# Optimization experiments

Measured on AMD Instinct MI355X. Metric: run time of the kernel, lower is better.

## Reference

```python
import jax, jax.numpy as jnp
import numpy as np

B, LQ, LKV, D = 8, 2048, 2048, 1024

def setup_inputs() -> dict:
    key = jax.random.key(0)
    k1, k2, k3, k4, k5, k6, k7 = jax.random.split(key, 7)
    s = 1.0 / np.sqrt(D)
    return {
        "query": jax.random.normal(k1, (B, LQ, D), jnp.float32),
        "key": jax.random.normal(k2, (B, LKV, D), jnp.float32),
        "value": jax.random.normal(k3, (B, LKV, D), jnp.float32),
        "Wq": jax.random.uniform(k4, (D, D), jnp.float32, -s, s),
        "bq": jax.random.uniform(k5, (D,), jnp.float32, -s, s),
        "Wk": jax.random.uniform(k6, (D, D), jnp.float32, -s, s),
        "bk": jax.random.uniform(k7, (D,), jnp.float32, -s, s),
        "scale_factor": 32,
        "dropout_p": 0,
    }

def reference(query, key, value, Wq, bq, Wk, bk, scale_factor, dropout_p):
    # q/k linear projections (torch Linear: x @ W^T + b); v is used raw per the source
    q = jnp.einsum("bld,ed->ble", query, Wq) + bq
    k = jnp.einsum("bld,ed->ble", key, Wk) + bk
    scores = jnp.einsum("bqd,bkd->bqk", q, k) / jnp.float32(scale_factor)
    attn = jax.nn.softmax(scores, axis=-1)
    # dropout_p == 0 -> identity (deterministic baseline)
    return jnp.einsum("bqk,bkd->bqd", attn, value)
```

## Files before the change

kernel.cpp:

```cpp
#include <hip/hip_runtime.h>

typedef __bf16 bf16;
typedef __attribute__((ext_vector_type(4))) __bf16 bf16x4;
typedef __attribute__((ext_vector_type(8))) __bf16 bf16x8;
typedef __attribute__((ext_vector_type(4))) float f32x4;

__device__ __forceinline__ void gload_lds16(const void* g, void* l) {
  __builtin_amdgcn_global_load_lds(
      (const __attribute__((address_space(1))) unsigned int*)(unsigned long long)g,
      (__attribute__((address_space(3))) unsigned int*)(unsigned long long)l,
      16, 0, 0);
}

__global__ void cast_f32_bf16(const float* __restrict__ in, bf16* __restrict__ out, int n4) {
  int i = blockIdx.x * blockDim.x + threadIdx.x;
  if (i >= n4) return;
  float4 v = reinterpret_cast<const float4*>(in)[i];
  bf16x4 o;
  o[0] = (bf16)v.x; o[1] = (bf16)v.y; o[2] = (bf16)v.z; o[3] = (bf16)v.w;
  reinterpret_cast<bf16x4*>(out)[i] = o;
}

__global__ void transpose_cast(const float* __restrict__ V, bf16* __restrict__ VT,
                               int rows, int cols) {
  __shared__ bf16 tile[64][65];
  const int b = blockIdx.z;
  const float* Vb = V + (long)b * rows * cols;
  bf16* VTb = VT + (long)b * rows * cols;
  const int d0 = blockIdx.x * 64;
  const int k0 = blockIdx.y * 64;
  const int t = threadIdx.x;
  const int r = t >> 4;
  const int c4 = (t & 15) * 4;
#pragma unroll
  for (int p = 0; p < 4; ++p) {
    float4 v = *reinterpret_cast<const float4*>(&Vb[(long)(k0 + p * 16 + r) * cols + d0 + c4]);
    tile[p * 16 + r][c4 + 0] = (bf16)v.x;
    tile[p * 16 + r][c4 + 1] = (bf16)v.y;
    tile[p * 16 + r][c4 + 2] = (bf16)v.z;
    tile[p * 16 + r][c4 + 3] = (bf16)v.w;
  }
  __syncthreads();
#pragma unroll
  for (int p = 0; p < 4; ++p) {
    const int dd = p * 16 + r;
    bf16x4 o;
    o[0] = tile[c4 + 0][dd];
    o[1] = tile[c4 + 1][dd];
    o[2] = tile[c4 + 2][dd];
    o[3] = tile[c4 + 3][dd];
    *reinterpret_cast<bf16x4*>(&VTb[(long)(d0 + dd) * rows + k0 + c4]) = o;
  }
}

__global__ void softmax_rows(bf16* __restrict__ S) {
  const long row = blockIdx.x;
  bf16* p = S + row * 2048;
  const int t = threadIdx.x;
  const int wid = t >> 6;
  const int lane = t & 63;
  bf16x8 v = *reinterpret_cast<bf16x8*>(p + t * 8);
  float f[8];
  float m = -3.0e38f;
#pragma unroll
  for (int j = 0; j < 8; ++j) { f[j] = (float)v[j]; m = fmaxf(m, f[j]); }
#pragma unroll
  for (int off = 32; off >= 1; off >>= 1) m = fmaxf(m, __shfl_xor(m, off));
  __shared__ float redm[4], reds[4];
  if (lane == 0) redm[wid] = m;
  __syncthreads();
  m = fmaxf(fmaxf(redm[0], redm[1]), fmaxf(redm[2], redm[3]));
  float s = 0.f;
#pragma unroll
  for (int j = 0; j < 8; ++j) { f[j] = __expf(f[j] - m); s += f[j]; }
#pragma unroll
  for (int off = 32; off >= 1; off >>= 1) s += __shfl_xor(s, off);
  if (lane == 0) reds[wid] = s;
  __syncthreads();
  s = reds[0] + reds[1] + reds[2] + reds[3];
  const float inv = 1.0f / s;
  bf16x8 o;
#pragma unroll
  for (int j = 0; j < 8; ++j) o[j] = (bf16)(f[j] * inv);
  *reinterpret_cast<bf16x8*>(p + t * 8) = o;
}

template <int MODE>
__global__ void gemm_bt(const bf16* __restrict__ A, const bf16* __restrict__ Bm,
                        const float* __restrict__ bias, void* __restrict__ Cvoid,
                        const int* __restrict__ scale_ptr,
                        int M, int N, int K, long sA, long sB, long sC) {
  __shared__ bf16 Alds[128][32];
  __shared__ bf16 Blds[128][32];
  const int t = threadIdx.x;
  const int lane = t & 63;
  const int wid = t >> 6;
  const int wm = wid >> 1;
  const int wn = wid & 1;

  const int gx = gridDim.x, gy = gridDim.y;
  const int nwg = gx * gy * gridDim.z;
  int id = blockIdx.x + gx * (blockIdx.y + gy * blockIdx.z);
  if ((nwg & 7) == 0) {
    const int cpx = nwg >> 3;
    id = (id & 7) * cpx + (id >> 3);
  }
  const int bx = id % gx;
  const int by = (id / gx) % gy;
  const int bz = id / (gx * gy);

  const bf16* Ab = A + (long)bz * sA;
  const bf16* Bb = Bm + (long)bz * sB;
  const int tile_m = by * 128;
  const int tile_n = bx * 128;

  const int r0 = t >> 2;
  const int kc0 = t & 3;
  const int sk = (kc0 ^ ((r0 >> 1) & 3)) * 8;
  const bf16* gA0 = Ab + (long)(tile_m + r0) * K + sk;
  const bf16* gA1 = gA0 + (long)64 * K;
  const bf16* gB0 = Bb + (long)(tile_n + r0) * K + sk;
  const bf16* gB1 = gB0 + (long)64 * K;
  bf16* lA0 = &Alds[0][0] + wid * 512;
  bf16* lA1 = lA0 + 2048;
  bf16* lB0 = &Blds[0][0] + wid * 512;
  bf16* lB1 = lB0 + 2048;

  const int frow = lane & 15;
  const int fkc = lane >> 4;
  const int pko = (fkc ^ ((frow >> 1) & 3)) * 8;
  const bf16* aFrag = &Alds[wm * 64 + frow][pko];
  const bf16* bFrag = &Blds[wn * 64 + frow][pko];

  f32x4 acc[4][4] = {};
  const int nk = K >> 5;
  for (int kt = 0; kt < nk; ++kt) {
    const int ko = kt * 32;
    gload_lds16(gA0 + ko, lA0);
    gload_lds16(gA1 + ko, lA1);
    gload_lds16(gB0 + ko, lB0);
    gload_lds16(gB1 + ko, lB1);
    __syncthreads();
    bf16x8 af[4], bfv[4];
#pragma unroll
    for (int i = 0; i < 4; ++i) {
      af[i] = *reinterpret_cast<const bf16x8*>(aFrag + i * 512);
      bfv[i] = *reinterpret_cast<const bf16x8*>(bFrag + i * 512);
    }
#pragma unroll
    for (int mi = 0; mi < 4; ++mi)
#pragma unroll
      for (int ni = 0; ni < 4; ++ni)
        acc[mi][ni] = __builtin_amdgcn_mfma_f32_16x16x32_bf16(af[mi], bfv[ni], acc[mi][ni], 0, 0, 0);
    __syncthreads();
  }

  float scl = 1.0f;
  if (MODE == 1) {
    const int iv = scale_ptr[0];
    const float fv = __int_as_float(iv);
    const float sv = (iv > 0 && iv < (1 << 20)) ? (float)iv : fv;
    scl = 1.0f / sv;
  }
  const int rb = tile_m + wm * 64 + ((lane >> 4) << 2);
  const int cb = tile_n + wn * 64 + (lane & 15);
  if (MODE == 2) {
    float* C = reinterpret_cast<float*>(Cvoid) + (long)bz * sC;
#pragma unroll
    for (int mi = 0; mi < 4; ++mi)
#pragma unroll
      for (int ni = 0; ni < 4; ++ni)
#pragma unroll
        for (int r = 0; r < 4; ++r)
          C[(long)(rb + mi * 16 + r) * N + (cb + ni * 16)] = acc[mi][ni][r];
  } else {
    bf16* C = reinterpret_cast<bf16*>(Cvoid) + (long)bz * sC;
#pragma unroll
    for (int ni = 0; ni < 4; ++ni) {
      const int col = cb + ni * 16;
      const float bv = (MODE == 0) ? bias[col] : 0.0f;
#pragma unroll
      for (int mi = 0; mi < 4; ++mi)
#pragma unroll
        for (int r = 0; r < 4; ++r)
          C[(long)(rb + mi * 16 + r) * N + col] = (bf16)(acc[mi][ni][r] * scl + bv);
    }
  }
}

extern "C" void kernel_launch(void* const* d_in, const int* in_sizes, int n_in,
                              void* d_out, int out_size, void* d_ws, size_t ws_size,
                              hipStream_t stream) {
  (void)in_sizes; (void)n_in; (void)out_size; (void)ws_size;
  const float* query = (const float*)d_in[0];
  const float* key   = (const float*)d_in[1];
  const float* value = (const float*)d_in[2];
  const float* Wq    = (const float*)d_in[3];
  const float* bq    = (const float*)d_in[4];
  const float* Wk    = (const float*)d_in[5];
  const float* bk    = (const float*)d_in[6];
  const int*   scale = (const int*)d_in[7];

  const int L = 2048, D = 1024;
  char* ws = (char*)d_ws;
  bf16* q_cast = (bf16*)ws;
  bf16* k_cast = q_cast + (long)16384 * 1024;
  bf16* S      = q_cast;
  bf16* Qp     = (bf16*)(ws + (size_t)67108864);
  bf16* Kp     = (bf16*)(ws + (size_t)100663296);
  bf16* VT     = (bf16*)(ws + (size_t)134217728);
  bf16* Wqb    = (bf16*)(ws + (size_t)167772160);
  bf16* Wkb    = (bf16*)(ws + (size_t)169869312);

  cast_f32_bf16<<<16384, 256, 0, stream>>>(query, q_cast, 4194304);
  cast_f32_bf16<<<16384, 256, 0, stream>>>(key,   k_cast, 4194304);
  cast_f32_bf16<<<1024,  256, 0, stream>>>(Wq, Wqb, 262144);
  cast_f32_bf16<<<1024,  256, 0, stream>>>(Wk, Wkb, 262144);
  transpose_cast<<<dim3(16, 32, 8), 256, 0, stream>>>(value, VT, 2048, 1024);

  gemm_bt<0><<<dim3(8, 128, 1), 256, 0, stream>>>(q_cast, Wqb, bq, Qp, nullptr,
                                                  16384, 1024, 1024, 0, 0, 0);
  gemm_bt<0><<<dim3(8, 128, 1), 256, 0, stream>>>(k_cast, Wkb, bk, Kp, nullptr,
                                                  16384, 1024, 1024, 0, 0, 0);
  gemm_bt<1><<<dim3(16, 16, 8), 256, 0, stream>>>(Qp, Kp, nullptr, S, scale,
                                                  2048, 2048, 1024,
                                                  (long)L * D, (long)L * D, (long)L * L);
  softmax_rows<<<16384, 256, 0, stream>>>(S);
  gemm_bt<2><<<dim3(8, 16, 8), 256, 0, stream>>>(S, VT, nullptr, d_out, nullptr,
                                                 2048, 1024, 2048,
                                                 (long)L * L, (long)D * L, (long)L * D);
}
```

Measured before the change: 324.3 us.

## Rewrite GEMM as 256x256 double-buffered pipelined kernel with 8 waves

Replaces the single-buffered 128x128x32 GEMM with a 256x256x64 tile using 512 threads, double-buffered LDS, and direct global-to-LDS async loads. The loads for the next k-tile are interleaved between quarters of the MFMA work, with explicit barriers, waitcnt and setprio. The goal is to hide global load latency behind compute and to raise arithmetic intensity per LDS byte. In exchange it uses 128KB of LDS per block and a large accumulator register footprint, which may limit occupancy. The grid swizzle now assumes the block count is divisible by 8.

After: 289.0 us. 1.12x faster.

```diff
diff --git a/kernel.cpp b/kernel.cpp
--- a/kernel.cpp
+++ b/kernel.cpp
@@ -85,23 +85,82 @@
   *reinterpret_cast<bf16x8*>(p + t * 8) = o;
 }
 
+
+#define BARRIER __builtin_amdgcn_s_barrier()
+#define LGKM0                                              \
+  do {                                                     \
+    asm volatile("s_waitcnt lgkmcnt(0)" ::: "memory");     \
+    __builtin_amdgcn_sched_barrier(0);                     \
+  } while (0)
+#define VM0                                                \
+  do {                                                     \
+    asm volatile("s_waitcnt vmcnt(0)" ::: "memory");       \
+    __builtin_amdgcn_sched_barrier(0);                     \
+  } while (0)
+
+#define STAGE_A(buf, ko)                                        \
+  {                                                             \
+    bf16* l_ = ldsd + (buf) * 32768;                            \
+    const bf16* g_ = gA + (ko);                                 \
+    gload_lds16(g_, l_);                                        \
+    gload_lds16(g_ + rK64, l_ + 4096);                          \
+    gload_lds16(g_ + rK128, l_ + 8192);                         \
+    gload_lds16(g_ + rK128 + rK64, l_ + 12288);                 \
+  }
+#define STAGE_B(buf, ko)                                        \
+  {                                                             \
+    bf16* l_ = ldsd + (buf) * 32768 + 16384;                    \
+    const bf16* g_ = gB + (ko);                                 \
+    gload_lds16(g_, l_);                                        \
+    gload_lds16(g_ + rK64, l_ + 4096);                          \
+    gload_lds16(g_ + rK128, l_ + 8192);                         \
+    gload_lds16(g_ + rK128 + rK64, l_ + 12288);                 \
+  }
+
+#define LOADA(buf, mq)                                                        \
+  {                                                                           \
+    const bf16* p_ = aBase + (buf) * 32768 + (mq) * 4096;                     \
+    _Pragma("unroll") for (int m_ = 0; m_ < 4; ++m_) {                        \
+      a[m_][0] = *reinterpret_cast<const bf16x8*>(p_ + m_ * 1024 + pk0);      \
+      a[m_][1] = *reinterpret_cast<const bf16x8*>(p_ + m_ * 1024 + pk1);      \
+    }                                                                         \
+  }
+#define LOADB(buf, nq)                                                        \
+  {                                                                           \
+    const bf16* p_ = bBase + (buf) * 32768 + (nq) * 2048;                     \
+    _Pragma("unroll") for (int n_ = 0; n_ < 2; ++n_) {                        \
+      b[(nq) * 2 + n_][0] = *reinterpret_cast<const bf16x8*>(p_ + n_ * 1024 + pk0); \
+      b[(nq) * 2 + n_][1] = *reinterpret_cast<const bf16x8*>(p_ + n_ * 1024 + pk1); \
+    }                                                                         \
+  }
+
+#define MFMAQ(mq, nq)                                                         \
+  _Pragma("unroll") for (int m_ = 0; m_ < 4; ++m_)                            \
+  _Pragma("unroll") for (int n_ = 0; n_ < 2; ++n_)                            \
+  _Pragma("unroll") for (int ks_ = 0; ks_ < 2; ++ks_)                         \
+      acc[(mq) * 4 + m_][(nq) * 2 + n_] =                                     \
+          __builtin_amdgcn_mfma_f32_16x16x32_bf16(                            \
+              a[m_][ks_], b[(nq) * 2 + n_][ks_],                              \
+              acc[(mq) * 4 + m_][(nq) * 2 + n_], 0, 0, 0);
+
 template <int MODE>
-__global__ void gemm_bt(const bf16* __restrict__ A, const bf16* __restrict__ Bm,
-                        const float* __restrict__ bias, void* __restrict__ Cvoid,
-                        const int* __restrict__ scale_ptr,
-                        int M, int N, int K, long sA, long sB, long sC) {
-  __shared__ bf16 Alds[128][32];
-  __shared__ bf16 Blds[128][32];
+__global__ __launch_bounds__(512, 2)
+void gemm_bt(const bf16* __restrict__ A, const bf16* __restrict__ Bm,
+             const float* __restrict__ bias, void* __restrict__ Cvoid,
+             const int* __restrict__ scale_ptr,
+             int M, int N, int K, long sA, long sB, long sC) {
+  __shared__ bf16 lds[2][2][2][128][64];
   const int t = threadIdx.x;
   const int lane = t & 63;
   const int wid = t >> 6;
-  const int wm = wid >> 1;
-  const int wn = wid & 1;
+  const int wm = wid >> 2;
+  const int wn = wid & 3;
+  (void)M;
 
   const int gx = gridDim.x, gy = gridDim.y;
   const int nwg = gx * gy * gridDim.z;
   int id = blockIdx.x + gx * (blockIdx.y + gy * blockIdx.z);
-  if ((nwg & 7) == 0) {
+  {
     const int cpx = nwg >> 3;
     id = (id & 7) * cpx + (id >> 3);
   }
@@ -111,49 +170,74 @@
 
   const bf16* Ab = A + (long)bz * sA;
   const bf16* Bb = Bm + (long)bz * sB;
-  const int tile_m = by * 128;
-  const int tile_n = bx * 128;
-
-  const int r0 = t >> 2;
-  const int kc0 = t & 3;
-  const int sk = (kc0 ^ ((r0 >> 1) & 3)) * 8;
-  const bf16* gA0 = Ab + (long)(tile_m + r0) * K + sk;
-  const bf16* gA1 = gA0 + (long)64 * K;
-  const bf16* gB0 = Bb + (long)(tile_n + r0) * K + sk;
-  const bf16* gB1 = gB0 + (long)64 * K;
-  bf16* lA0 = &Alds[0][0] + wid * 512;
-  bf16* lA1 = lA0 + 2048;
-  bf16* lB0 = &Blds[0][0] + wid * 512;
-  bf16* lB1 = lB0 + 2048;
+  const int tile_m = by * 256;
+  const int tile_n = bx * 256;
+
+  const int srow = t >> 3;
+  const int skc = t & 7;
+  const int soff = ((skc ^ (srow & 7)) << 3);
+  const bf16* gA = Ab + (long)(tile_m + srow) * K + soff;
+  const bf16* gB = Bb + (long)(tile_n + srow) * K + soff;
+  const long rK64 = (long)K << 6;
+  const long rK128 = (long)K << 7;
+  bf16* const ldsd = &lds[0][0][0][0][0] + wid * 512;
 
   const int frow = lane & 15;
-  const int fkc = lane >> 4;
-  const int pko = (fkc ^ ((frow >> 1) & 3)) * 8;
-  const bf16* aFrag = &Alds[wm * 64 + frow][pko];
-  const bf16* bFrag = &Blds[wn * 64 + frow][pko];
-
-  f32x4 acc[4][4] = {};
-  const int nk = K >> 5;
-  for (int kt = 0; kt < nk; ++kt) {
-    const int ko = kt * 32;
-    gload_lds16(gA0 + ko, lA0);
-    gload_lds16(gA1 + ko, lA1);
-    gload_lds16(gB0 + ko, lB0);
-    gload_lds16(gB1 + ko, lB1);
-    __syncthreads();
-    bf16x8 af[4], bfv[4];
-#pragma unroll
-    for (int i = 0; i < 4; ++i) {
-      af[i] = *reinterpret_cast<const bf16x8*>(aFrag + i * 512);
-      bfv[i] = *reinterpret_cast<const bf16x8*>(bFrag + i * 512);
-    }
-#pragma unroll
-    for (int mi = 0; mi < 4; ++mi)
-#pragma unroll
-      for (int ni = 0; ni < 4; ++ni)
-        acc[mi][ni] = __builtin_amdgcn_mfma_f32_16x16x32_bf16(af[mi], bfv[ni], acc[mi][ni], 0, 0, 0);
-    __syncthreads();
-  }
+  const int pk0 = (((lane >> 4) ^ (lane & 7))) << 3;
+  const int pk1 = (((4 | (lane >> 4)) ^ (lane & 7))) << 3;
+  const bf16* aBase = &lds[0][0][wm][frow][0];
+  const bf16* bBase = &lds[0][1][wn >> 1][(wn & 1) * 64 + frow][0];
+
+  bf16x8 a[4][2], b[4][2];
+  f32x4 acc[8][4] = {};
+
+  STAGE_A(0, 0)
+  STAGE_B(0, 0)
+  VM0;
+  BARRIER;
+
+  const int NK = K >> 6;
+  int c = 0;
+  for (int kt = 0; kt < NK - 1; ++kt, c ^= 1) {
+    const long ko = (long)(kt + 1) << 6;
+    LOADA(c, 0)
+    LOADB(c, 0)
+    STAGE_A(c ^ 1, ko)
+    BARRIER;
+    LGKM0;
+    __builtin_amdgcn_s_setprio(1);
+    MFMAQ(0, 0)
+    __builtin_amdgcn_s_setprio(0);
+    BARRIER;
+    LOADB(c, 1)
+    STAGE_B(c ^ 1, ko)
+    BARRIER;
+    LGKM0;
+    __builtin_amdgcn_s_setprio(1);
+    MFMAQ(0, 1)
+    __builtin_amdgcn_s_setprio(0);
+    BARRIER;
+    LOADA(c, 1)
+    BARRIER;
+    LGKM0;
+    __builtin_amdgcn_s_setprio(1);
+    MFMAQ(1, 0)
+    __builtin_amdgcn_s_setprio(0);
+    BARRIER;
+    VM0;
+    BARRIER;
+    __builtin_amdgcn_s_setprio(1);
+    MFMAQ(1, 1)
+    __builtin_amdgcn_s_setprio(0);
+  }
+  LOADA(c, 0)
+  LOADB(c, 0)
+  LOADB(c, 1)
+  MFMAQ(0, 0)
+  MFMAQ(0, 1)
+  LOADA(c, 1)
+  MFMAQ(1, 0)
+  MFMAQ(1, 1)
 
   float scl = 1.0f;
   if (MODE == 1) {
@@ -162,28 +246,28 @@
     const float sv = (iv > 0 && iv < (1 << 20)) ? (float)iv : fv;
     scl = 1.0f / sv;
   }
-  const int rb = tile_m + wm * 64 + ((lane >> 4) << 2);
+  const int rb = tile_m + wm * 128 + ((lane >> 4) << 2);
   const int cb = tile_n + wn * 64 + (lane & 15);
   if (MODE == 2) {
     float* C = reinterpret_cast<float*>(Cvoid) + (long)bz * sC;
 #pragma unroll
-    for (int mi = 0; mi < 4; ++mi)
-#pragma unroll
-      for (int ni = 0; ni < 4; ++ni)
+    for (int mf = 0; mf < 8; ++mf)
+#pragma unroll
+      for (int nf = 0; nf < 4; ++nf)
 #pragma unroll
         for (int r = 0; r < 4; ++r)
-          C[(long)(rb + mi * 16 + r) * N + (cb + ni * 16)] = acc[mi][ni][r];
+          C[(long)(rb + mf * 16 + r) * N + (cb + nf * 16)] = acc[mf][nf][r];
   } else {
     bf16* C = reinterpret_cast<bf16*>(Cvoid) + (long)bz * sC;
 #pragma unroll
-    for (int ni = 0; ni < 4; ++ni) {
-      const int col = cb + ni * 16;
+    for (int nf = 0; nf < 4; ++nf) {
+      const int col = cb + nf * 16;
       const float bv = (MODE == 0) ? bias[col] : 0.0f;
 #pragma unroll
-      for (int mi = 0; mi < 4; ++mi)
+      for (int mf = 0; mf < 8; ++mf)
 #pragma unroll
         for (int r = 0; r < 4; ++r)
-          C[(long)(rb + mi * 16 + r) * N + col] = (bf16)(acc[mi][ni][r] * scl + bv);
+          C[(long)(rb + mf * 16 + r) * N + col] = (bf16)(acc[mf][nf][r] * scl + bv);
     }
   }
 }
@@ -218,15 +302,15 @@
   cast_f32_bf16<<<1024,  256, 0, stream>>>(Wk, Wkb, 262144);
   transpose_cast<<<dim3(16, 32, 8), 256, 0, stream>>>(value, VT, 2048, 1024);
 
-  gemm_bt<0><<<dim3(8, 128, 1), 256, 0, stream>>>(q_cast, Wqb, bq, Qp, nullptr,
-                                                  16384, 1024, 1024, 0, 0, 0);
-  gemm_bt<0><<<dim3(8, 128, 1), 256, 0, stream>>>(k_cast, Wkb, bk, Kp, nullptr,
-                                                  16384, 1024, 1024, 0, 0, 0);
-  gemm_bt<1><<<dim3(16, 16, 8), 256, 0, stream>>>(Qp, Kp, nullptr, S, scale,
-                                                  2048, 2048, 1024,
-                                                  (long)L * D, (long)L * D, (long)L * L);
+  gemm_bt<0><<<dim3(4, 64, 1), 512, 0, stream>>>(q_cast, Wqb, bq, Qp, nullptr,
+                                                 16384, 1024, 1024, 0, 0, 0);
+  gemm_bt<0><<<dim3(4, 64, 1), 512, 0, stream>>>(k_cast, Wkb, bk, Kp, nullptr,
+                                                 16384, 1024, 1024, 0, 0, 0);
+  gemm_bt<1><<<dim3(8, 8, 8), 512, 0, stream>>>(Qp, Kp, nullptr, S, scale,
+                                                2048, 2048, 1024,
+                                                (long)L * D, (long)L * D, (long)L * L);
   softmax_rows<<<16384, 256, 0, stream>>>(S);
-  gemm_bt<2><<<dim3(8, 16, 8), 256, 0, stream>>>(S, VT, nullptr, d_out, nullptr,
-                                                 2048, 1024, 2048,
-                                                 (long)L * L, (long)D * L, (long)L * D);
-}
+  gemm_bt<2><<<dim3(4, 8, 8), 512, 0, stream>>>(S, VT, nullptr, d_out, nullptr,
+                                                2048, 1024, 2048,
+                                                (long)L * L, (long)D * L, (long)L * D);
+}
```

## Double-buffer LDS in GEMM, widen tile to 128x256, merge Q/K projections

Applied to the files above, without the earlier changes.

The GEMM kernel now uses 512 threads with a 128x256 output tile and double-buffered LDS. The next K-slice is prefetched with global_load_lds while the current one is consumed, so only one barrier remains per iteration. The two separate Q and K projection launches are merged into a single batched launch that picks the bias by batch index. Together these aim to hide global-load latency and raise B-tile reuse, at the cost of more LDS per block (48KB) and possibly lower occupancy.

New measurement: 298.2 us. -8.0%, faster.

```diff
diff --git a/kernel.cpp b/kernel.cpp
--- a/kernel.cpp
+++ b/kernel.cpp
@@ -85,23 +85,46 @@
   *reinterpret_cast<bf16x8*>(p + t * 8) = o;
 }
 
+
+#define STAGE(buf, ko)                          \
+  {                                             \
+    bf16* lA_ = ldsA + (buf) * 12288;           \
+    bf16* lB_ = ldsB + (buf) * 12288;           \
+    gload_lds16(gA + (ko), lA_);                \
+    gload_lds16(gB + (ko), lB_);                \
+    gload_lds16(gB + (ko) + rK128, lB_ + 4096); \
+  }
+
+#define LOADA(buf)                                                             \
+  _Pragma("unroll") for (int m_ = 0; m_ < 4; ++m_)                             \
+      a[m_] = *reinterpret_cast<const bf16x8*>(aB + (buf) * 12288 + m_ * 512);
+#define LOADB(buf)                                                             \
+  _Pragma("unroll") for (int n_ = 0; n_ < 4; ++n_)                             \
+      b[n_] = *reinterpret_cast<const bf16x8*>(bB + (buf) * 12288 + n_ * 512);
+
+#define MFMAP                                                                  \
+  _Pragma("unroll") for (int m_ = 0; m_ < 4; ++m_)                             \
+  _Pragma("unroll") for (int n_ = 0; n_ < 4; ++n_)                             \
+      acc[m_][n_] = __builtin_amdgcn_mfma_f32_16x16x32_bf16(                   \
+          a[m_], b[n_], acc[m_][n_], 0, 0, 0);
+
 template <int MODE>
-__global__ void gemm_bt(const bf16* __restrict__ A, const bf16* __restrict__ Bm,
-                        const float* __restrict__ bias, void* __restrict__ Cvoid,
-                        const int* __restrict__ scale_ptr,
-                        int M, int N, int K, long sA, long sB, long sC) {
-  __shared__ bf16 Alds[128][32];
-  __shared__ bf16 Blds[128][32];
+__global__ __launch_bounds__(512, 4)
+void gemm_bt(const bf16* __restrict__ A, const bf16* __restrict__ Bm,
+             const float* __restrict__ bias0, const float* __restrict__ bias1,
+             void* __restrict__ Cvoid, const int* __restrict__ scale_ptr,
+             int N, int K, long sA, long sB, long sC) {
+  __shared__ bf16 lds[2][12288];
   const int t = threadIdx.x;
   const int lane = t & 63;
   const int wid = t >> 6;
-  const int wm = wid >> 1;
-  const int wn = wid & 1;
+  const int wm = wid >> 2;
+  const int wn = wid & 3;
 
   const int gx = gridDim.x, gy = gridDim.y;
   const int nwg = gx * gy * gridDim.z;
   int id = blockIdx.x + gx * (blockIdx.y + gy * blockIdx.z);
-  if ((nwg & 7) == 0) {
+  {
     const int cpx = nwg >> 3;
     id = (id & 7) * cpx + (id >> 3);
   }
@@ -112,48 +135,39 @@
   const bf16* Ab = A + (long)bz * sA;
   const bf16* Bb = Bm + (long)bz * sB;
   const int tile_m = by * 128;
-  const int tile_n = bx * 128;
-
-  const int r0 = t >> 2;
-  const int kc0 = t & 3;
-  const int sk = (kc0 ^ ((r0 >> 1) & 3)) * 8;
-  const bf16* gA0 = Ab + (long)(tile_m + r0) * K + sk;
-  const bf16* gA1 = gA0 + (long)64 * K;
-  const bf16* gB0 = Bb + (long)(tile_n + r0) * K + sk;
-  const bf16* gB1 = gB0 + (long)64 * K;
-  bf16* lA0 = &Alds[0][0] + wid * 512;
-  bf16* lA1 = lA0 + 2048;
-  bf16* lB0 = &Blds[0][0] + wid * 512;
-  bf16* lB1 = lB0 + 2048;
+  const int tile_n = bx * 256;
+
+  const int srow = t >> 2;
+  const int soff = (((t & 3) ^ ((t >> 3) & 3)) << 3);
+  const bf16* gA = Ab + (long)(tile_m + srow) * K + soff;
+  const bf16* gB = Bb + (long)(tile_n + srow) * K + soff;
+  const long rK128 = (long)K << 7;
+  bf16* const ldsA = &lds[0][0] + wid * 512;
+  bf16* const ldsB = &lds[0][4096] + wid * 512;
 
   const int frow = lane & 15;
-  const int fkc = lane >> 4;
-  const int pko = (fkc ^ ((frow >> 1) & 3)) * 8;
-  const bf16* aFrag = &Alds[wm * 64 + frow][pko];
-  const bf16* bFrag = &Blds[wn * 64 + frow][pko];
-
+  const int pko = (((lane >> 4) ^ ((lane >> 1) & 3)) << 3);
+  const bf16* aB = &lds[0][0] + (wm * 64 + frow) * 32 + pko;
+  const bf16* bB = &lds[0][4096] + (wn * 64 + frow) * 32 + pko;
+
+  bf16x8 a[4], b[4];
   f32x4 acc[4][4] = {};
-  const int nk = K >> 5;
-  for (int kt = 0; kt < nk; ++kt) {
-    const int ko = kt * 32;
-    gload_lds16(gA0 + ko, lA0);
-    gload_lds16(gA1 + ko, lA1);
-    gload_lds16(gB0 + ko, lB0);
-    gload_lds16(gB1 + ko, lB1);
+
+  STAGE(0, 0)
+  __syncthreads();
+
+  const int NK = K >> 5;
+  int c = 0;
+  for (int kt = 0; kt < NK - 1; ++kt, c ^= 1) {
+    STAGE(c ^ 1, (long)(kt + 1) << 5)
+    LOADB(c)
+    LOADA(c)
+    MFMAP
     __syncthreads();
-    bf16x8 af[4], bfv[4];
-#pragma unroll
-    for (int i = 0; i < 4; ++i) {
-      af[i] = *reinterpret_cast<const bf16x8*>(aFrag + i * 512);
-      bfv[i] = *reinterpret_cast<const bf16x8*>(bFrag + i * 512);
-    }
-#pragma unroll
-    for (int mi = 0; mi < 4; ++mi)
-#pragma unroll
-      for (int ni = 0; ni < 4; ++ni)
-        acc[mi][ni] = __builtin_amdgcn_mfma_f32_16x16x32_bf16(af[mi], bfv[ni], acc[mi][ni], 0, 0, 0);
-    __syncthreads();
-  }
+  }
+  LOADB(c)
+  LOADA(c)
+  MFMAP
 
   float scl = 1.0f;
   if (MODE == 1) {
@@ -167,23 +181,24 @@
   if (MODE == 2) {
     float* C = reinterpret_cast<float*>(Cvoid) + (long)bz * sC;
 #pragma unroll
-    for (int mi = 0; mi < 4; ++mi)
-#pragma unroll
-      for (int ni = 0; ni < 4; ++ni)
+    for (int mf = 0; mf < 4; ++mf)
+#pragma unroll
+      for (int nf = 0; nf < 4; ++nf)
 #pragma unroll
         for (int r = 0; r < 4; ++r)
-          C[(long)(rb + mi * 16 + r) * N + (cb + ni * 16)] = acc[mi][ni][r];
+          C[(long)(rb + mf * 16 + r) * N + (cb + nf * 16)] = acc[mf][nf][r];
   } else {
     bf16* C = reinterpret_cast<bf16*>(Cvoid) + (long)bz * sC;
-#pragma unroll
-    for (int ni = 0; ni < 4; ++ni) {
-      const int col = cb + ni * 16;
+    const float* bias = (MODE == 0) ? (bz ? bias1 : bias0) : nullptr;
+#pragma unroll
+    for (int nf = 0; nf < 4; ++nf) {
+      const int col = cb + nf * 16;
       const float bv = (MODE == 0) ? bias[col] : 0.0f;
 #pragma unroll
-      for (int mi = 0; mi < 4; ++mi)
+      for (int mf = 0; mf < 4; ++mf)
 #pragma unroll
         for (int r = 0; r < 4; ++r)
-          C[(long)(rb + mi * 16 + r) * N + col] = (bf16)(acc[mi][ni][r] * scl + bv);
+          C[(long)(rb + mf * 16 + r) * N + col] = (bf16)(acc[mf][nf][r] * scl + bv);
     }
   }
 }
@@ -218,15 +233,14 @@
   cast_f32_bf16<<<1024,  256, 0, stream>>>(Wk, Wkb, 262144);
   transpose_cast<<<dim3(16, 32, 8), 256, 0, stream>>>(value, VT, 2048, 1024);
 
-  gemm_bt<0><<<dim3(8, 128, 1), 256, 0, stream>>>(q_cast, Wqb, bq, Qp, nullptr,
-                                                  16384, 1024, 1024, 0, 0, 0);
-  gemm_bt<0><<<dim3(8, 128, 1), 256, 0, stream>>>(k_cast, Wkb, bk, Kp, nullptr,
-                                                  16384, 1024, 1024, 0, 0, 0);
-  gemm_bt<1><<<dim3(16, 16, 8), 256, 0, stream>>>(Qp, Kp, nullptr, S, scale,
-                                                  2048, 2048, 1024,
-                                                  (long)L * D, (long)L * D, (long)L * L);
+  gemm_bt<0><<<dim3(4, 128, 2), 512, 0, stream>>>(q_cast, Wqb, bq, bk, Qp, nullptr,
+                                                  1024, 1024,
+                                                  16777216L, 1048576L, 16777216L);
+  gemm_bt<1><<<dim3(8, 16, 8), 512, 0, stream>>>(Qp, Kp, nullptr, nullptr, S, scale,
+                                                 2048, 1024,
+                                                 (long)L * D, (long)L * D, (long)L * L);
   softmax_rows<<<16384, 256, 0, stream>>>(S);
-  gemm_bt<2><<<dim3(8, 16, 8), 256, 0, stream>>>(S, VT, nullptr, d_out, nullptr,
-                                                 2048, 1024, 2048,
+  gemm_bt<2><<<dim3(4, 16, 8), 512, 0, stream>>>(S, VT, nullptr, nullptr, d_out, nullptr,
+                                                 1024, 2048,
                                                  (long)L * L, (long)D * L, (long)L * D);
 }
```
